# Kernel tuning notes

Hardware: AMD Instinct MI355X
Metric: run time of the kernel (lower is better)

## Reference

```python
import jax, jax.numpy as jnp
import numpy as np

N_NODES = 8   # chain DAG 0->1->...->7
B = 2048      # n_samples
T_STEPS = 8   # end_wind
Z_DIM = 32    # latent_dim // 2
EMB = 8       # emb_dim
GRU_H = 24
HID = 64


def setup_inputs() -> dict:
    key = jax.random.key(0)
    ks = jax.random.split(key, 20)
    def rn(k, shape, scale=0.1):
        return jax.random.normal(k, shape, jnp.float32) * scale
    return {
        "z": jax.random.normal(ks[0], (N_NODES, B, T_STEPS, Z_DIM), jnp.float32),
        "cond_w1": rn(ks[1], (N_NODES, 32, 1)),
        "cond_b1": rn(ks[2], (N_NODES, 32)),
        "cond_w2": rn(ks[3], (N_NODES, EMB, 32)),
        "cond_b2": rn(ks[4], (N_NODES, EMB)),
        "proj_w": rn(ks[5], (N_NODES, GRU_H, Z_DIM + 2 * EMB)),  # node 0 uses first 40 cols
        "proj_b": rn(ks[6], (N_NODES, GRU_H)),
        "gru_proj_w": rn(ks[7], (GRU_H, GRU_H)),
        "gru_proj_b": rn(ks[8], (GRU_H,)),
        "gru_wih": rn(ks[9], (N_NODES, 2, 3 * GRU_H, GRU_H)),
        "gru_whh": rn(ks[10], (N_NODES, 2, 3 * GRU_H, GRU_H)),
        "gru_bih": rn(ks[11], (N_NODES, 2, 3 * GRU_H)),
        "gru_bhh": rn(ks[12], (N_NODES, 2, 3 * GRU_H)),
        "cm_w1": rn(ks[13], (N_NODES, HID, GRU_H)),
        "cm_b1": rn(ks[14], (N_NODES, HID)),
        "cm_w2": rn(ks[15], (N_NODES, HID, HID)),
        "cm_b2": rn(ks[16], (N_NODES, HID)),
        "cm_w3": rn(ks[17], (N_NODES, 1, HID)),
        "cm_b3": rn(ks[18], (N_NODES, 1)),
        "end_wind": T_STEPS,
    }


def _leaky(x):
    return jnp.where(x >= 0, x, 0.01 * x)  # nn.LeakyReLU default slope


def _gru_layer(x, wih, whh, bih, bhh):
    """torch nn.GRU single layer, batch_first. x: [B, L, H] -> [B, L, H]."""
    h0 = jnp.zeros((x.shape[0], GRU_H), x.dtype)
    def step(h, xt):
        gi = xt @ wih.T + bih            # [B, 3H], gate order r, z, n
        gh = h @ whh.T + bhh
        i_r, i_z, i_n = jnp.split(gi, 3, axis=-1)
        h_r, h_z, h_n = jnp.split(gh, 3, axis=-1)
        r = jax.nn.sigmoid(i_r + h_r)
        zg = jax.nn.sigmoid(i_z + h_z)
        n = jnp.tanh(i_n + r * h_n)
        hn = (1.0 - zg) * n + zg * h
        return hn, hn
    _, ys = jax.lax.scan(step, h0, jnp.swapaxes(x, 0, 1))
    return jnp.swapaxes(ys, 0, 1)


def _forward(z, cond_w1, cond_b1, cond_w2, cond_b2, proj_w, proj_b,
             gru_proj_w, gru_proj_b, gru_wih, gru_whh, gru_bih, gru_bhh,
             cm_w1, cm_b1, cm_w2, cm_b2, cm_w3, cm_b3, end_wind):
    n_nodes, bsz = z.shape[0], z.shape[1]
    dt = z.dtype

    def cond_net(n, x):  # x: [B, L, 1] -> [B, L, EMB]
        h = jax.nn.relu(x @ cond_w1[n].T + cond_b1[n])
        return h @ cond_w2[n].T + cond_b2[n]

    def pipeline(n, z_mod):  # decode_pipeline: proj -> leaky -> gru_proj -> 2-layer GRU -> CausalMap
        w = proj_w[n][:, : z_mod.shape[-1]]
        h = _leaky(z_mod @ w.T + proj_b[n])
        g = h @ gru_proj_w.T + gru_proj_b
        y = _gru_layer(g, gru_wih[n, 0], gru_whh[n, 0], gru_bih[n, 0], gru_bhh[n, 0])
        y = _gru_layer(y, gru_wih[n, 1], gru_whh[n, 1], gru_bih[n, 1], gru_bhh[n, 1])
        d = jax.nn.relu(y @ cm_w1[n].T + cm_b1[n])
        d = jax.nn.relu(d @ cm_w2[n].T + cm_b2[n])
        return d @ cm_w3[n].T + cm_b3[n]  # [B, L, 1]

    decoded = [None] * n_nodes
    reals = [[] for _ in range(n_nodes)]
    for idx in range(end_wind):
        # chain DAG: in-degree grouping (deg 0 = node 0, deg 1 = nodes 1..7 in order)
        # coincides with node order 0..N-1.
        for node in range(n_nodes):
            z_mod = z[node][:, : idx + 1]                       # [B, idx+1, Z_DIM]
            if idx != 0:
                emb_self = cond_net(node, decoded[node])        # [B, idx, EMB]
                emb_self = jnp.concatenate(
                    [emb_self, jnp.zeros((bsz, 1, EMB), dt)], axis=1)
            else:
                emb_self = jnp.zeros((bsz, 1, EMB), dt)
            z_mod = jnp.concatenate([z_mod, emb_self], axis=2)
            if node > 0:  # single predecessor node-1, already decoded this idx
                if idx != 0:
                    emb_p = cond_net(node - 1, decoded[node - 1])  # [B, idx+1, EMB]
                else:
                    emb_p = jnp.zeros((bsz, 1, EMB), dt)
                z_mod = jnp.concatenate([z_mod, emb_p], axis=2)
            d = pipeline(node, z_mod)                           # [B, idx+1, 1]
            decoded[node] = d
            reals[node].append(d[:, idx:idx + 1, 0])
    # [B, T, N]
    return jnp.stack([jnp.concatenate(r, axis=1) for r in reals], axis=-1)


def reference(z, cond_w1, cond_b1, cond_w2, cond_b2, proj_w, proj_b,
              gru_proj_w, gru_proj_b, gru_wih, gru_whh, gru_bih, gru_bhh,
              cm_w1, cm_b1, cm_w2, cm_b2, cm_w3, cm_b3, end_wind):
    return _forward(z, cond_w1, cond_b1, cond_w2, cond_b2, proj_w, proj_b,
                    gru_proj_w, gru_proj_b, gru_wih, gru_whh, gru_bih, gru_bhh,
                    cm_w1, cm_b1, cm_w2, cm_b2, cm_w3, cm_b3, int(end_wind))
```

## Files before the change

kernel.cpp:

```cpp
#include <hip/hip_runtime.h>


#define NT 64
#define SYNC() asm volatile("s_waitcnt lgkmcnt(0)" ::: "memory")

__device__ __forceinline__ float sigm(float x) { return 1.0f / (1.0f + __expf(-x)); }
__device__ __forceinline__ float tanh_fast(float x) {
  x = fminf(15.0f, fmaxf(-15.0f, x));
  float e = __expf(2.0f * x);
  return (e - 1.0f) / (e + 1.0f);
}
__device__ __forceinline__ float leaky(float x) { return x >= 0.0f ? x : 0.01f * x; }

template <int N4>
__device__ __forceinline__ float dotv2(const float* __restrict__ w, const float* h) {
  const float4* w4 = reinterpret_cast<const float4*>(w);
  const float4* h4 = reinterpret_cast<const float4*>(h);
  float a0 = 0.0f, a1 = 0.0f;
#pragma unroll
  for (int i = 0; i < N4; i += 2) {
    float4 x0 = w4[i], y0 = h4[i];
    float4 x1 = w4[i + 1], y1 = h4[i + 1];
    a0 = fmaf(x0.x, y0.x, a0); a0 = fmaf(x0.y, y0.y, a0);
    a0 = fmaf(x0.z, y0.z, a0); a0 = fmaf(x0.w, y0.w, a0);
    a1 = fmaf(x1.x, y1.x, a1); a1 = fmaf(x1.y, y1.y, a1);
    a1 = fmaf(x1.z, y1.z, a1); a1 = fmaf(x1.w, y1.w, a1);
  }
  return a0 + a1;
}

template <int N4>
__device__ __forceinline__ float dotv4(const float* __restrict__ w, const float* h) {
  const float4* w4 = reinterpret_cast<const float4*>(w);
  const float4* h4 = reinterpret_cast<const float4*>(h);
  float a0 = 0.0f, a1 = 0.0f, a2 = 0.0f, a3 = 0.0f;
#pragma unroll
  for (int i = 0; i < N4; i += 4) {
    float4 x0 = w4[i], y0 = h4[i];
    float4 x1 = w4[i + 1], y1 = h4[i + 1];
    float4 x2 = w4[i + 2], y2 = h4[i + 2];
    float4 x3 = w4[i + 3], y3 = h4[i + 3];
    a0 = fmaf(x0.x, y0.x, a0); a0 = fmaf(x0.y, y0.y, a0);
    a0 = fmaf(x0.z, y0.z, a0); a0 = fmaf(x0.w, y0.w, a0);
    a1 = fmaf(x1.x, y1.x, a1); a1 = fmaf(x1.y, y1.y, a1);
    a1 = fmaf(x1.z, y1.z, a1); a1 = fmaf(x1.w, y1.w, a1);
    a2 = fmaf(x2.x, y2.x, a2); a2 = fmaf(x2.y, y2.y, a2);
    a2 = fmaf(x2.z, y2.z, a2); a2 = fmaf(x2.w, y2.w, a2);
    a3 = fmaf(x3.x, y3.x, a3); a3 = fmaf(x3.y, y3.y, a3);
    a3 = fmaf(x3.w, y3.w, a3); a3 = fmaf(x3.z, y3.z, a3);
  }
  return (a0 + a1) + (a2 + a3);
}

__device__ __forceinline__ void load_gates_w(
    const float* __restrict__ wih, const float* __restrict__ bih,
    int lane, int rowB, float4 WA[6], float4 WB[6], float& bA, float& bB) {
  const float4* wa = reinterpret_cast<const float4*>(wih + (size_t)lane * 24);
  const float4* wb = reinterpret_cast<const float4*>(wih + (size_t)rowB * 24);
#pragma unroll
  for (int i = 0; i < 6; ++i) { WA[i] = wa[i]; WB[i] = wb[i]; }
  bA = bih[lane]; bB = bih[rowB];
}

__device__ __forceinline__ void load_rec_w(
    const float* __restrict__ whh, const float* __restrict__ bhh,
    int jq, int half, float4 Wr[3], float4 Wz[3], float4 Wn[3],
    float& bR, float& bZ, float& bN) {
  const float4* wr = reinterpret_cast<const float4*>(whh + jq * 24 + half * 12);
  const float4* wz = reinterpret_cast<const float4*>(whh + (24 + jq) * 24 + half * 12);
  const float4* wn = reinterpret_cast<const float4*>(whh + (48 + jq) * 24 + half * 12);
#pragma unroll
  for (int i = 0; i < 3; ++i) { Wr[i] = wr[i]; Wz[i] = wz[i]; Wn[i] = wn[i]; }
  bR = half ? 0.0f : bhh[jq];
  bZ = half ? 0.0f : bhh[24 + jq];
  bN = half ? 0.0f : bhh[48 + jq];
}

__device__ __forceinline__ void gates_comp(
    const float4 WA[6], const float4 WB[6], float bA, float bB,
    const float* srcp, float* s_gi, int L, int lane) {
  int t = 0;
#pragma unroll 1
  for (; t + 1 < L; t += 2) {
    const float4* h0 = reinterpret_cast<const float4*>(srcp + t * 24);
    const float4* h1 = reinterpret_cast<const float4*>(srcp + t * 24 + 24);
    float a0 = bA, a1 = bA, c0 = bB, c1 = bB;
#pragma unroll
    for (int i = 0; i < 6; ++i) {
      float4 p = h0[i], q = h1[i], A = WA[i], Bv = WB[i];
      a0 = fmaf(A.x, p.x, a0); a0 = fmaf(A.y, p.y, a0);
      a0 = fmaf(A.z, p.z, a0); a0 = fmaf(A.w, p.w, a0);
      a1 = fmaf(A.x, q.x, a1); a1 = fmaf(A.y, q.y, a1);
      a1 = fmaf(A.z, q.z, a1); a1 = fmaf(A.w, q.w, a1);
      c0 = fmaf(Bv.x, p.x, c0); c0 = fmaf(Bv.y, p.y, c0);
      c0 = fmaf(Bv.z, p.z, c0); c0 = fmaf(Bv.w, p.w, c0);
      c1 = fmaf(Bv.x, q.x, c1); c1 = fmaf(Bv.y, q.y, c1);
      c1 = fmaf(Bv.z, q.z, c1); c1 = fmaf(Bv.w, q.w, c1);
    }
    s_gi[t * 72 + lane] = a0;
    s_gi[t * 72 + 72 + lane] = a1;
    if (lane < 8) {
      s_gi[t * 72 + 64 + lane] = c0;
      s_gi[t * 72 + 136 + lane] = c1;
    }
  }
  if (t < L) {
    const float4* h0 = reinterpret_cast<const float4*>(srcp + t * 24);
    float a0 = bA, c0 = bB;
#pragma unroll
    for (int i = 0; i < 6; ++i) {
      float4 p = h0[i], A = WA[i], Bv = WB[i];
      a0 = fmaf(A.x, p.x, a0); a0 = fmaf(A.y, p.y, a0);
      a0 = fmaf(A.z, p.z, a0); a0 = fmaf(A.w, p.w, a0);
      c0 = fmaf(Bv.x, p.x, c0); c0 = fmaf(Bv.y, p.y, c0);
      c0 = fmaf(Bv.z, p.z, c0); c0 = fmaf(Bv.w, p.w, c0);
    }
    s_gi[t * 72 + lane] = a0;
    if (lane < 8) s_gi[t * 72 + 64 + lane] = c0;
  }
}

__device__ __forceinline__ void rec_comp(
    const float4 Wr[3], const float4 Wz[3], const float4 Wn[3],
    float bR, float bZ, float bN,
    const float* s_gi, float* s_hid, float* s_y, int L, int lane, int jq, int half) {
  if (lane < 24) s_hid[lane] = 0.0f;
  int cur = 0;
#pragma unroll 1
  for (int t = 0; t < L; ++t) {
    const float4* hp = reinterpret_cast<const float4*>(s_hid + cur * 24 + half * 12);
    float gr = bR, gz = bZ, gn = bN;
#pragma unroll
    for (int i = 0; i < 3; ++i) {
      float4 hh = hp[i];
      gr = fmaf(Wr[i].x, hh.x, gr); gr = fmaf(Wr[i].y, hh.y, gr);
      gr = fmaf(Wr[i].z, hh.z, gr); gr = fmaf(Wr[i].w, hh.w, gr);
      gz = fmaf(Wz[i].x, hh.x, gz); gz = fmaf(Wz[i].y, hh.y, gz);
      gz = fmaf(Wz[i].z, hh.z, gz); gz = fmaf(Wz[i].w, hh.w, gz);
      gn = fmaf(Wn[i].x, hh.x, gn); gn = fmaf(Wn[i].y, hh.y, gn);
      gn = fmaf(Wn[i].z, hh.z, gn); gn = fmaf(Wn[i].w, hh.w, gn);
    }
    gr += __shfl_xor(gr, 32);
    gz += __shfl_xor(gz, 32);
    gn += __shfl_xor(gn, 32);
    const float* gi = s_gi + t * 72;
    float r   = sigm(gi[jq] + gr);
    float zg  = sigm(gi[24 + jq] + gz);
    float nn2 = tanh_fast(gi[48 + jq] + r * gn);
    float hold = s_hid[cur * 24 + jq];
    float hnew = fmaf(zg, hold - nn2, nn2);
    if (lane < 24) {
      s_hid[(cur ^ 1) * 24 + lane] = hnew;
      s_y[t * 24 + lane] = hnew;
    }
    cur ^= 1;
  }
}

__global__ void fuse_kernel(const float* __restrict__ gru_wih,
                            const float* __restrict__ gru_bih,
                            const float* __restrict__ gpw,
                            const float* __restrict__ gpb,
                            float* __restrict__ fw, float* __restrict__ fb) {
  const int n = blockIdx.x;
  const int tid = threadIdx.x;
  const float* w = gru_wih + (size_t)(n * 2) * 1728;
  for (int it = tid; it < 1728; it += 64) {
    int r = it / 24, k = it - r * 24;
    float acc = 0.0f;
#pragma unroll
    for (int j = 0; j < 24; ++j) acc = fmaf(w[r * 24 + j], gpw[j * 24 + k], acc);
    fw[(size_t)n * 1728 + it] = acc;
  }
  if (tid < 72 + 0) {
    for (int r = tid; r < 72; r += 64) {
      float acc = gru_bih[(n * 2) * 72 + r];
#pragma unroll
      for (int j = 0; j < 24; ++j) acc = fmaf(w[r * 24 + j], gpb[j], acc);
      fb[n * 72 + r] = acc;
    }
  }
}

__global__ __launch_bounds__(NT, 2) void tcm_kernel(
    const float* __restrict__ z,
    const float* __restrict__ cond_w1, const float* __restrict__ cond_b1,
    const float* __restrict__ cond_w2, const float* __restrict__ cond_b2,
    const float* __restrict__ proj_w, const float* __restrict__ proj_b,
    const float* __restrict__ gru_wih, const float* __restrict__ gru_whh,
    const float* __restrict__ gru_bih, const float* __restrict__ gru_bhh,
    const float* __restrict__ cm_w1, const float* __restrict__ cm_b1,
    const float* __restrict__ cm_w2, const float* __restrict__ cm_b2,
    const float* __restrict__ cm_w3, const float* __restrict__ cm_b3,
    const int* __restrict__ endw,
    const float* __restrict__ fw, const float* __restrict__ fb,
    float* __restrict__ out, int Btot) {
  __shared__ __align__(16) float lds[4832];
  float* s_e   = lds;
  float* s_h   = lds + 128;
  float* s_gi  = lds + 320;
  float* s_y   = lds + 896;
  float* s_hid = lds + 1088;
  float* s_d1  = lds + 1136;
  float* s_d2  = lds + 1680;
  float* s_dd  = lds + 2224;
  float* s_ch  = lds + 2240;
  float* s_emb = lds + 2528;
  float* s_pz  = lds + 3040;
  float* s_zz  = lds + 4576;

  const int lane = threadIdx.x;
  const int b = blockIdx.x;
  const int T = endw[0];
  const int jm = lane & 31;
  const int half = lane >> 5;
  const int jq = jm < 24 ? jm : 0;
  const int rowB = 64 + (lane & 7);

#pragma unroll 1
  for (int idx = 0; idx < T; ++idx) {
    const int L = idx + 1;
#pragma unroll 1
    for (int n = 0; n < 8; ++n) {
      const float* wih1 = gru_wih + (size_t)(n * 2 + 1) * 1728;
      const float* whh0 = gru_whh + (size_t)(n * 2) * 1728;
      const float* whh1 = whh0 + 1728;
      const float* bih1 = gru_bih + (n * 2 + 1) * 72;
      const float* bhh0 = gru_bhh + (n * 2) * 72;
      const float* bhh1 = bhh0 + 72;

      float4 WA[6], WB[6]; float bA, bB;
      load_gates_w(fw + (size_t)n * 1728, fb + n * 72, lane, rowB, WA, WB, bA, bB);

      if (idx == 0) {
        const float4* z4 = reinterpret_cast<const float4*>(
            z + ((size_t)n * Btot + b) * 8 * 32);
        reinterpret_cast<float4*>(s_zz)[lane] = z4[lane];
        SYNC();
#pragma unroll 1
        for (int it = lane; it < 192; it += NT) {
          int t = it / 24, j = it - t * 24;
          s_pz[n * 192 + t * 24 + j] =
              proj_b[n * 24 + j] +
              dotv2<8>(proj_w + (size_t)(n * 24 + j) * 48, s_zz + t * 32);
        }
      }
#pragma unroll 1
      for (int it = lane; it < L * 16; it += NT) {
        int t = it >> 4, c = it & 15;
        float v = 0.0f;
        if (c < 8) {
          if (t < idx) v = s_emb[n * 64 + t * 8 + c];
        } else {
          if (n > 0 && idx > 0) v = s_emb[(n - 1) * 64 + t * 8 + (c - 8)];
        }
        s_e[t * 16 + c] = v;
      }
      SYNC();
#pragma unroll 1
      for (int it = lane; it < L * 24; it += NT) {
        int t = it / 24, j = it - t * 24;
        float acc = s_pz[n * 192 + t * 24 + j] +
                    dotv2<4>(proj_w + (size_t)(n * 24 + j) * 48 + 32, s_e + t * 16);
        s_h[t * 24 + j] = leaky(acc);
      }
      SYNC();
      float4 Wr[3], Wz[3], Wn[3]; float bR, bZ, bN;
      load_rec_w(whh0, bhh0, jq, half, Wr, Wz, Wn, bR, bZ, bN);
      gates_comp(WA, WB, bA, bB, s_h, s_gi, L, lane);
      SYNC();
      float4 WA1[6], WB1[6]; float bA1, bB1;
      load_gates_w(wih1, bih1, lane, rowB, WA1, WB1, bA1, bB1);
      rec_comp(Wr, Wz, Wn, bR, bZ, bN, s_gi, s_hid, s_y, L, lane, jq, half);
      SYNC();
      float4 Wr1[3], Wz1[3], Wn1[3]; float bR1, bZ1, bN1;
      load_rec_w(whh1, bhh1, jq, half, Wr1, Wz1, Wn1, bR1, bZ1, bN1);
      gates_comp(WA1, WB1, bA1, bB1, s_y, s_gi, L, lane);
      SYNC();
      float4 C1[6];
      {
        const float4* p = reinterpret_cast<const float4*>(
            cm_w1 + (size_t)(n * 64 + lane) * 24);
#pragma unroll
        for (int i = 0; i < 6; ++i) C1[i] = p[i];
      }
      const float c1b = cm_b1[n * 64 + lane];
      rec_comp(Wr1, Wz1, Wn1, bR1, bZ1, bN1, s_gi, s_hid, s_y, L, lane, jq, half);
      SYNC();
      float4 C2[16];
      {
        const float4* p = reinterpret_cast<const float4*>(
            cm_w2 + (size_t)(n * 64 + lane) * 64);
#pragma unroll
        for (int i = 0; i < 16; ++i) C2[i] = p[i];
      }
      const float c2b = cm_b2[n * 64 + lane];
      {
        int t = 0;
#pragma unroll 1
        for (; t + 1 < L; t += 2) {
          const float4* y0 = reinterpret_cast<const float4*>(s_y + t * 24);
          const float4* y1 = reinterpret_cast<const float4*>(s_y + t * 24 + 24);
          float a0 = c1b, a1 = c1b;
#pragma unroll
          for (int i = 0; i < 6; ++i) {
            float4 pp = y0[i], q = y1[i], W = C1[i];
            a0 = fmaf(W.x, pp.x, a0); a0 = fmaf(W.y, pp.y, a0);
            a0 = fmaf(W.z, pp.z, a0); a0 = fmaf(W.w, pp.w, a0);
            a1 = fmaf(W.x, q.x, a1); a1 = fmaf(W.y, q.y, a1);
            a1 = fmaf(W.z, q.z, a1); a1 = fmaf(W.w, q.w, a1);
          }
          s_d1[t * 68 + lane] = fmaxf(a0, 0.0f);
          s_d1[t * 68 + 68 + lane] = fmaxf(a1, 0.0f);
        }
        if (t < L) {
          float acc = c1b;
          const float4* y0 = reinterpret_cast<const float4*>(s_y + t * 24);
#pragma unroll
          for (int i = 0; i < 6; ++i) {
            float4 pp = y0[i], W = C1[i];
            acc = fmaf(W.x, pp.x, acc); acc = fmaf(W.y, pp.y, acc);
            acc = fmaf(W.z, pp.z, acc); acc = fmaf(W.w, pp.w, acc);
          }
          s_d1[t * 68 + lane] = fmaxf(acc, 0.0f);
        }
      }
      SYNC();
      {
        int t = 0;
#pragma unroll 1
        for (; t + 1 < L; t += 2) {
          const float4* d0 = reinterpret_cast<const float4*>(s_d1 + t * 68);
          const float4* d1 = reinterpret_cast<const float4*>(s_d1 + t * 68 + 68);
          float a0 = c2b, a1 = 0.0f, c0 = c2b, c1 = 0.0f;
#pragma unroll
          for (int i = 0; i < 16; i += 2) {
            float4 W0 = C2[i], W1 = C2[i + 1];
            float4 p0 = d0[i], p1 = d0[i + 1], q0 = d1[i], q1 = d1[i + 1];
            a0 = fmaf(W0.x, p0.x, a0); a0 = fmaf(W0.y, p0.y, a0);
            a0 = fmaf(W0.z, p0.z, a0); a0 = fmaf(W0.w, p0.w, a0);
            a1 = fmaf(W1.x, p1.x, a1); a1 = fmaf(W1.y, p1.y, a1);
            a1 = fmaf(W1.z, p1.z, a1); a1 = fmaf(W1.w, p1.w, a1);
            c0 = fmaf(W0.x, q0.x, c0); c0 = fmaf(W0.y, q0.y, c0);
            c0 = fmaf(W0.z, q0.z, c0); c0 = fmaf(W0.w, q0.w, c0);
            c1 = fmaf(W1.x, q1.x, c1); c1 = fmaf(W1.y, q1.y, c1);
            c1 = fmaf(W1.z, q1.z, c1); c1 = fmaf(W1.w, q1.w, c1);
          }
          s_d2[t * 68 + lane] = fmaxf(a0 + a1, 0.0f);
          s_d2[t * 68 + 68 + lane] = fmaxf(c0 + c1, 0.0f);
        }
        if (t < L) {
          const float4* d0 = reinterpret_cast<const float4*>(s_d1 + t * 68);
          float a0 = c2b, a1 = 0.0f;
#pragma unroll
          for (int i = 0; i < 16; i += 2) {
            float4 W0 = C2[i], W1 = C2[i + 1];
            float4 p0 = d0[i], p1 = d0[i + 1];
            a0 = fmaf(W0.x, p0.x, a0); a0 = fmaf(W0.y, p0.y, a0);
            a0 = fmaf(W0.z, p0.z, a0); a0 = fmaf(W0.w, p0.w, a0);
            a1 = fmaf(W1.x, p1.x, a1); a1 = fmaf(W1.y, p1.y, a1);
            a1 = fmaf(W1.z, p1.z, a1); a1 = fmaf(W1.w, p1.w, a1);
          }
          s_d2[t * 68 + lane] = fmaxf(a0 + a1, 0.0f);
        }
      }
      SYNC();
      if (lane < L) {
        int t = lane;
        float dv = cm_b3[n] + dotv4<16>(cm_w3 + n * 64, s_d2 + t * 68);
        s_dd[t] = dv;
        if (t == idx)
          out[((size_t)b * T + idx) * 8 + n] = dv;
      }
      SYNC();
#pragma unroll 1
      for (int it = lane; it < L * 32; it += NT) {
        int t = it >> 5, k = it & 31;
        s_ch[t * 36 + k] =
            fmaxf(fmaf(s_dd[t], cond_w1[n * 32 + k], cond_b1[n * 32 + k]), 0.0f);
      }
      SYNC();
      if (lane < L * 8) {
        int t = lane >> 3, c = lane & 7;
        s_emb[n * 64 + t * 8 + c] =
            cond_b2[n * 8 + c] +
            dotv2<8>(cond_w2 + (size_t)(n * 8 + c) * 32, s_ch + t * 36);
      }
      SYNC();
    }
  }
}

extern "C" void kernel_launch(void* const* d_in, const int* in_sizes, int n_in,
                              void* d_out, int out_size, void* d_ws, size_t ws_size,
                              hipStream_t stream) {
  const float* z       = (const float*)d_in[0];
  const float* cond_w1 = (const float*)d_in[1];
  const float* cond_b1 = (const float*)d_in[2];
  const float* cond_w2 = (const float*)d_in[3];
  const float* cond_b2 = (const float*)d_in[4];
  const float* proj_w  = (const float*)d_in[5];
  const float* proj_b  = (const float*)d_in[6];
  const float* gpw     = (const float*)d_in[7];
  const float* gpb     = (const float*)d_in[8];
  const float* gru_wih = (const float*)d_in[9];
  const float* gru_whh = (const float*)d_in[10];
  const float* gru_bih = (const float*)d_in[11];
  const float* gru_bhh = (const float*)d_in[12];
  const float* cm_w1   = (const float*)d_in[13];
  const float* cm_b1   = (const float*)d_in[14];
  const float* cm_w2   = (const float*)d_in[15];
  const float* cm_b2   = (const float*)d_in[16];
  const float* cm_w3   = (const float*)d_in[17];
  const float* cm_b3   = (const float*)d_in[18];
  const int*   endw    = (const int*)d_in[19];
  float* out = (float*)d_out;

  int Btot = in_sizes[0] / (8 * 8 * 32);

  float* fw = (float*)d_ws;
  float* fb = fw + 8 * 1728;

  fuse_kernel<<<8, 64, 0, stream>>>(gru_wih, gru_bih, gpw, gpb, fw, fb);

  tcm_kernel<<<Btot, NT, 0, stream>>>(
      z, cond_w1, cond_b1, cond_w2, cond_b2, proj_w, proj_b,
      gru_wih, gru_whh, gru_bih, gru_bhh, cm_w1, cm_b1, cm_w2, cm_b2,
      cm_w3, cm_b3, endw, fw, fb, out, Btot);
}
```

Measured before the change: 870.5 us.

## Interleave the two GRU layers' recurrences step by step in one loop

Fuses the two stacked GRU layers into a single wavefront loop. Layer-0 step t is interleaved with layer-1's input-gate row and recurrent step t-1, so the two independent dependency chains can overlap. This removes a full separate recurrence pass, a bulk gates pass and their barriers, at the cost of extra live registers and reusing the s_d1 and s_zz LDS regions for layer-1 gates and hidden state. The launch bounds are also relaxed from 2 to 1 waves per SIMD so the compiler can allocate more registers, which may lower occupancy.

```diff
diff --git a/kernel.cpp b/kernel.cpp
--- a/kernel.cpp
+++ b/kernel.cpp
@@ -120,40 +120,50 @@
   }
 }
 
-__device__ __forceinline__ void rec_comp(
+__device__ __forceinline__ void gates_row(
+    const float4 WA[6], const float4 WB[6], float bA, float bB,
+    const float* src_row, float* gi_row, int lane) {
+  const float4* h0 = reinterpret_cast<const float4*>(src_row);
+  float a0 = bA, c0 = bB;
+#pragma unroll
+  for (int i = 0; i < 6; ++i) {
+    float4 p = h0[i], A = WA[i], Bv = WB[i];
+    a0 = fmaf(A.x, p.x, a0); a0 = fmaf(A.y, p.y, a0);
+    a0 = fmaf(A.z, p.z, a0); a0 = fmaf(A.w, p.w, a0);
+    c0 = fmaf(Bv.x, p.x, c0); c0 = fmaf(Bv.y, p.y, c0);
+    c0 = fmaf(Bv.z, p.z, c0); c0 = fmaf(Bv.w, p.w, c0);
+  }
+  gi_row[lane] = a0;
+  if (lane < 8) gi_row[64 + lane] = c0;
+}
+
+__device__ __forceinline__ void rec_step(
     const float4 Wr[3], const float4 Wz[3], const float4 Wn[3],
-    float bR, float bZ, float bN,
-    const float* s_gi, float* s_hid, float* s_y, int L, int lane, int jq, int half) {
-  if (lane < 24) s_hid[lane] = 0.0f;
-  int cur = 0;
-#pragma unroll 1
-  for (int t = 0; t < L; ++t) {
-    const float4* hp = reinterpret_cast<const float4*>(s_hid + cur * 24 + half * 12);
-    float gr = bR, gz = bZ, gn = bN;
-#pragma unroll
-    for (int i = 0; i < 3; ++i) {
-      float4 hh = hp[i];
-      gr = fmaf(Wr[i].x, hh.x, gr); gr = fmaf(Wr[i].y, hh.y, gr);
-      gr = fmaf(Wr[i].z, hh.z, gr); gr = fmaf(Wr[i].w, hh.w, gr);
-      gz = fmaf(Wz[i].x, hh.x, gz); gz = fmaf(Wz[i].y, hh.y, gz);
-      gz = fmaf(Wz[i].z, hh.z, gz); gz = fmaf(Wz[i].w, hh.w, gz);
-      gn = fmaf(Wn[i].x, hh.x, gn); gn = fmaf(Wn[i].y, hh.y, gn);
-      gn = fmaf(Wn[i].z, hh.z, gn); gn = fmaf(Wn[i].w, hh.w, gn);
-    }
-    gr += __shfl_xor(gr, 32);
-    gz += __shfl_xor(gz, 32);
-    gn += __shfl_xor(gn, 32);
-    const float* gi = s_gi + t * 72;
-    float r   = sigm(gi[jq] + gr);
-    float zg  = sigm(gi[24 + jq] + gz);
-    float nn2 = tanh_fast(gi[48 + jq] + r * gn);
-    float hold = s_hid[cur * 24 + jq];
-    float hnew = fmaf(zg, hold - nn2, nn2);
-    if (lane < 24) {
-      s_hid[(cur ^ 1) * 24 + lane] = hnew;
-      s_y[t * 24 + lane] = hnew;
-    }
-    cur ^= 1;
+    float bR, float bZ, float bN, const float* gi_row,
+    float* s_hid, int cur, float* y_row, int lane, int jq, int half) {
+  const float4* hp = reinterpret_cast<const float4*>(s_hid + cur * 24 + half * 12);
+  float gr = bR, gz = bZ, gn = bN;
+#pragma unroll
+  for (int i = 0; i < 3; ++i) {
+    float4 hh = hp[i];
+    gr = fmaf(Wr[i].x, hh.x, gr); gr = fmaf(Wr[i].y, hh.y, gr);
+    gr = fmaf(Wr[i].z, hh.z, gr); gr = fmaf(Wr[i].w, hh.w, gr);
+    gz = fmaf(Wz[i].x, hh.x, gz); gz = fmaf(Wz[i].y, hh.y, gz);
+    gz = fmaf(Wz[i].z, hh.z, gz); gz = fmaf(Wz[i].w, hh.w, gz);
+    gn = fmaf(Wn[i].x, hh.x, gn); gn = fmaf(Wn[i].y, hh.y, gn);
+    gn = fmaf(Wn[i].z, hh.z, gn); gn = fmaf(Wn[i].w, hh.w, gn);
+  }
+  gr += __shfl_xor(gr, 32);
+  gz += __shfl_xor(gz, 32);
+  gn += __shfl_xor(gn, 32);
+  float r   = sigm(gi_row[jq] + gr);
+  float zg  = sigm(gi_row[24 + jq] + gz);
+  float nn2 = tanh_fast(gi_row[48 + jq] + r * gn);
+  float hold = s_hid[cur * 24 + jq];
+  float hnew = fmaf(zg, hold - nn2, nn2);
+  if (lane < 24) {
+    s_hid[(cur ^ 1) * 24 + lane] = hnew;
+    y_row[lane] = hnew;
   }
 }
 
@@ -172,17 +182,15 @@
     for (int j = 0; j < 24; ++j) acc = fmaf(w[r * 24 + j], gpw[j * 24 + k], acc);
     fw[(size_t)n * 1728 + it] = acc;
   }
-  if (tid < 72 + 0) {
-    for (int r = tid; r < 72; r += 64) {
-      float acc = gru_bih[(n * 2) * 72 + r];
-#pragma unroll
-      for (int j = 0; j < 24; ++j) acc = fmaf(w[r * 24 + j], gpb[j], acc);
-      fb[n * 72 + r] = acc;
-    }
-  }
-}
-
-__global__ __launch_bounds__(NT, 2) void tcm_kernel(
+  for (int r = tid; r < 72; r += 64) {
+    float acc = gru_bih[(n * 2) * 72 + r];
+#pragma unroll
+    for (int j = 0; j < 24; ++j) acc = fmaf(w[r * 24 + j], gpb[j], acc);
+    fb[n * 72 + r] = acc;
+  }
+}
+
+__global__ __launch_bounds__(NT, 1) void tcm_kernel(
     const float* __restrict__ z,
     const float* __restrict__ cond_w1, const float* __restrict__ cond_b1,
     const float* __restrict__ cond_w2, const float* __restrict__ cond_b2,
@@ -196,18 +204,20 @@
     const float* __restrict__ fw, const float* __restrict__ fb,
     float* __restrict__ out, int Btot) {
   __shared__ __align__(16) float lds[4832];
-  float* s_e   = lds;
-  float* s_h   = lds + 128;
-  float* s_gi  = lds + 320;
-  float* s_y   = lds + 896;
-  float* s_hid = lds + 1088;
-  float* s_d1  = lds + 1136;
-  float* s_d2  = lds + 1680;
-  float* s_dd  = lds + 2224;
-  float* s_ch  = lds + 2240;
-  float* s_emb = lds + 2528;
-  float* s_pz  = lds + 3040;
-  float* s_zz  = lds + 4576;
+  float* s_e    = lds;
+  float* s_h    = lds + 128;
+  float* s_gi0  = lds + 320;
+  float* s_y    = lds + 896;
+  float* s_hidA = lds + 1088;
+  float* s_d1   = lds + 1136;
+  float* s_d2   = lds + 1680;
+  float* s_dd   = lds + 2224;
+  float* s_ch   = lds + 2240;
+  float* s_emb  = lds + 2528;
+  float* s_pz   = lds + 3040;
+  float* s_zz   = lds + 4576;
+  float* s_gi1  = lds + 1136;
+  float* s_hidB = lds + 4576;
 
   const int lane = threadIdx.x;
   const int b = blockIdx.x;
@@ -265,17 +275,36 @@
         s_h[t * 24 + j] = leaky(acc);
       }
       SYNC();
-      float4 Wr[3], Wz[3], Wn[3]; float bR, bZ, bN;
-      load_rec_w(whh0, bhh0, jq, half, Wr, Wz, Wn, bR, bZ, bN);
-      gates_comp(WA, WB, bA, bB, s_h, s_gi, L, lane);
+      float4 Wr0[3], Wz0[3], Wn0[3]; float bR0, bZ0, bN0;
+      load_rec_w(whh0, bhh0, jq, half, Wr0, Wz0, Wn0, bR0, bZ0, bN0);
+      gates_comp(WA, WB, bA, bB, s_h, s_gi0, L, lane);
       SYNC();
       float4 WA1[6], WB1[6]; float bA1, bB1;
       load_gates_w(wih1, bih1, lane, rowB, WA1, WB1, bA1, bB1);
-      rec_comp(Wr, Wz, Wn, bR, bZ, bN, s_gi, s_hid, s_y, L, lane, jq, half);
-      SYNC();
       float4 Wr1[3], Wz1[3], Wn1[3]; float bR1, bZ1, bN1;
       load_rec_w(whh1, bhh1, jq, half, Wr1, Wz1, Wn1, bR1, bZ1, bN1);
-      gates_comp(WA1, WB1, bA1, bB1, s_y, s_gi, L, lane);
+      {
+        if (lane < 24) { s_hidA[lane] = 0.0f; s_hidB[lane] = 0.0f; }
+        int curA = 0, curB = 0;
+        rec_step(Wr0, Wz0, Wn0, bR0, bZ0, bN0, s_gi0, s_hidA, curA,
+                 s_y, lane, jq, half);
+        curA ^= 1;
+#pragma unroll 1
+        for (int t = 1; t < L; ++t) {
+          rec_step(Wr0, Wz0, Wn0, bR0, bZ0, bN0, s_gi0 + t * 72, s_hidA, curA,
+                   s_y + t * 24, lane, jq, half);
+          curA ^= 1;
+          gates_row(WA1, WB1, bA1, bB1, s_y + (t - 1) * 24,
+                    s_gi1 + (t - 1) * 72, lane);
+          rec_step(Wr1, Wz1, Wn1, bR1, bZ1, bN1, s_gi1 + (t - 1) * 72,
+                   s_hidB, curB, s_y + (t - 1) * 24, lane, jq, half);
+          curB ^= 1;
+        }
+        gates_row(WA1, WB1, bA1, bB1, s_y + (L - 1) * 24,
+                  s_gi1 + (L - 1) * 72, lane);
+        rec_step(Wr1, Wz1, Wn1, bR1, bZ1, bN1, s_gi1 + (L - 1) * 72,
+                 s_hidB, curB, s_y + (L - 1) * 24, lane, jq, half);
+      }
       SYNC();
       float4 C1[6];
       {
@@ -285,8 +314,6 @@
         for (int i = 0; i < 6; ++i) C1[i] = p[i];
       }
       const float c1b = cm_b1[n * 64 + lane];
-      rec_comp(Wr1, Wz1, Wn1, bR1, bZ1, bN1, s_gi, s_hid, s_y, L, lane, jq, half);
-      SYNC();
       float4 C2[16];
       {
         const float4* p = reinterpret_cast<const float4*>(
```

After: 892.4 us. 1.03x slower.
